# Kernel optimization log

Measured on AMD Instinct MI355X. Metric: run time of the kernel, lower is better.

Reference implementation:

```python
import jax, jax.numpy as jnp
import numpy as np

N = 100_000   # nodes
E = 1_600_000 # edges (avg degree 16)
D = 128       # dim == dim_out
NEG_SLOPE = 0.2  # PyG GATConv default


def setup_inputs() -> dict:
    key = jax.random.key(0)
    ks = jax.random.split(key, 11)
    s = 1.0 / np.sqrt(D)
    return {
        "x": jax.random.normal(ks[0], (N, D), jnp.float32),
        "edge_index": jax.random.randint(ks[1], (2, E), 0, N, jnp.int32),
        "W1": jax.random.normal(ks[2], (D, D), jnp.float32) * s,
        "a_src1": jax.random.normal(ks[3], (D,), jnp.float32) * s,
        "a_dst1": jax.random.normal(ks[4], (D,), jnp.float32) * s,
        "b1": jnp.zeros((D,), jnp.float32),
        "W2": jax.random.normal(ks[5], (D, D), jnp.float32) * s,
        "a_src2": jax.random.normal(ks[6], (D,), jnp.float32) * s,
        "a_dst2": jax.random.normal(ks[7], (D,), jnp.float32) * s,
        "b2": jnp.zeros((D,), jnp.float32),
    }


def gat_conv(x, W, a_src, a_dst, b, src, dst, n):
    # PyG GATConv, heads=1: message flows src (j) -> dst (i)
    h = x @ W                              # [n, d]
    al_src = h @ a_src                     # per-node src attention logit
    al_dst = h @ a_dst                     # per-node dst attention logit
    e = jax.nn.leaky_relu(al_src[src] + al_dst[dst], NEG_SLOPE)  # [E']
    # softmax over incoming edges of each destination node (segment softmax)
    m = jax.ops.segment_max(e, dst, num_segments=n)
    e = jnp.exp(e - m[dst])
    z = jax.ops.segment_sum(e, dst, num_segments=n)
    alpha = e / z[dst]                     # [E']
    out = jax.ops.segment_sum(h[src] * alpha[:, None], dst, num_segments=n)
    return out + b


def reference(x, edge_index, W1, a_src1, a_dst1, b1, W2, a_src2, a_dst2, b2):
    n = x.shape[0]
    loop = jnp.arange(n, dtype=edge_index.dtype)
    src = jnp.concatenate([edge_index[0], loop])  # add_self_loops=True
    dst = jnp.concatenate([edge_index[1], loop])
    h = gat_conv(x, W1, a_src1, a_dst1, b1, src, dst, n)
    # self_loops=True -> residual=False; dropout in eval mode = identity
    return gat_conv(h, W2, a_src2, a_dst2, b2, src, dst, n)
```

## Files before the change

### kernel.cpp

```cpp
#include <hip/hip_runtime.h>
#include <hip/hip_bf16.h>
#include <math.h>

#define D 128
#define LRELU_SLOPE 0.2f
#define BSH 9
#define BSZ 512
#define SC_CHUNK 16384

typedef __attribute__((ext_vector_type(8))) short bf16x8;
typedef __attribute__((ext_vector_type(4))) float f32x4;

__device__ __forceinline__ float lrelu(float x){ return x > 0.f ? x : LRELU_SLOPE * x; }

__device__ __forceinline__ unsigned short bf16_rn(float x){
  unsigned int u = __float_as_uint(x);
  return (unsigned short)((u + 0x7FFFu + ((u >> 16) & 1u)) >> 16);
}
__device__ __forceinline__ float bf16_lo_f(unsigned int u){ return __uint_as_float(u << 16); }
__device__ __forceinline__ float bf16_hi_f(unsigned int u){ return __uint_as_float(u & 0xFFFF0000u); }

__global__ __launch_bounds__(1024) void bucket_count_kernel(const int* __restrict__ dst, int E,
    int* __restrict__ bcnt, int nbuck){
  __shared__ int h[256];
  int t = threadIdx.x;
  if (t < 256) h[t] = 0;
  __syncthreads();
  for (int e = blockIdx.x*1024 + t; e < E; e += gridDim.x*1024)
    atomicAdd(&h[dst[e] >> BSH], 1);
  __syncthreads();
  if (t < nbuck && h[t]) atomicAdd(&bcnt[t], h[t]);
}

__global__ __launch_bounds__(256) void bucket_scan_kernel(const int* __restrict__ bcnt,
    int* __restrict__ bbase, int* __restrict__ bcur, int nbuck, int E){
  __shared__ int s[256];
  int t = threadIdx.x;
  int v = (t < nbuck) ? bcnt[t] : 0;
  s[t] = v;
  __syncthreads();
  #pragma unroll
  for (int d = 1; d < 256; d <<= 1){
    int add = (t >= d) ? s[t-d] : 0;
    __syncthreads();
    s[t] += add;
    __syncthreads();
  }
  if (t < nbuck){ int b = s[t] - v; bbase[t] = b; bcur[t] = b; }
  if (t == 0) bbase[nbuck] = E;
}

__global__ __launch_bounds__(1024) void bucket_scatter_kernel(const int* __restrict__ src,
    const int* __restrict__ dst, int E, int* __restrict__ bcur,
    unsigned int* __restrict__ ebuf, int nbuck){
  __shared__ int h[256];
  __shared__ int cb[256];
  int t = threadIdx.x;
  int base = blockIdx.x * SC_CHUNK;
  int end = base + SC_CHUNK; if (end > E) end = E;
  if (t < 256) h[t] = 0;
  __syncthreads();
  for (int e = base + t; e < end; e += 1024)
    atomicAdd(&h[dst[e] >> BSH], 1);
  __syncthreads();
  if (t < nbuck){
    cb[t] = h[t] ? atomicAdd(&bcur[t], h[t]) : 0;
    h[t] = 0;
  }
  __syncthreads();
  for (int e = base + t; e < end; e += 1024){
    int d = dst[e];
    int b = d >> BSH;
    int lpos = atomicAdd(&h[b], 1);
    ebuf[cb[b] + lpos] = ((unsigned int)src[e] << BSH) | (unsigned int)(d & (BSZ-1));
  }
}

__global__ __launch_bounds__(256) void bucket_csr_kernel(const unsigned int* __restrict__ ebuf,
    const int* __restrict__ bbase, int* __restrict__ row_ptr, int* __restrict__ col,
    int n, int nbuck){
  __shared__ int c[512];
  __shared__ int ps[256];
  int b = blockIdx.x;
  int t = threadIdx.x;
  int base = bbase[b], end = bbase[b+1];
  c[t] = 0; c[t+256] = 0;
  __syncthreads();
  for (int i = base + t; i < end; i += 256)
    atomicAdd(&c[ebuf[i] & (BSZ-1)], 1);
  __syncthreads();
  int a0 = c[2*t], a1 = c[2*t+1];
  int pair = a0 + a1;
  ps[t] = pair;
  __syncthreads();
  #pragma unroll
  for (int d = 1; d < 256; d <<= 1){
    int add = (t >= d) ? ps[t-d] : 0;
    __syncthreads();
    ps[t] += add;
    __syncthreads();
  }
  int excl = ps[t] - pair;
  __syncthreads();
  int lo = b << BSH;
  int g0 = lo + 2*t, g1 = g0 + 1;
  if (g0 < n) row_ptr[g0] = base + excl;
  if (g1 < n) row_ptr[g1] = base + excl + a0;
  c[2*t]   = excl;
  c[2*t+1] = excl + a0;
  __syncthreads();
  for (int i = base + t; i < end; i += 256){
    unsigned int p = ebuf[i];
    int dlo = p & (BSZ-1);
    int pos = base + atomicAdd(&c[dlo], 1);
    col[pos] = (int)(p >> BSH);
  }
  if (b == 0 && t == 0) row_ptr[n] = bbase[nbuck];
}

__global__ __launch_bounds__(256) void wsplit_kernel(const float* __restrict__ W,
    unsigned short* __restrict__ Whf, unsigned short* __restrict__ Wlf){
  int t = blockIdx.x*256 + threadIdx.x;
  int k  = t >> 7;
  int nn = t & 127;
  float w = W[t];
  unsigned short h = bf16_rn(w);
  float whf = __uint_as_float(((unsigned int)h) << 16);
  unsigned short l = bf16_rn(w - whf);
  int kc = k >> 5, l4 = (k >> 3) & 3, e = k & 7;
  int cf = nn >> 4, l15 = nn & 15;
  int idx = ((kc*8 + cf)*64 + l4*16 + l15)*8 + e;
  Whf[idx] = h; Wlf[idx] = l;
}

__global__ __launch_bounds__(64) void wa_kernel(const float* __restrict__ W,
    const float* __restrict__ a_src, const float* __restrict__ a_dst,
    float* __restrict__ wa_s, float* __restrict__ wa_d){
  int task = blockIdx.x;
  int row = task & 127;
  const float* a = (task >> 7) ? a_dst : a_src;
  int l = threadIdx.x;
  float2 v = ((const float2*)(W + row*D))[l];
  float p = v.x*a[2*l] + v.y*a[2*l+1];
  #pragma unroll
  for (int off = 32; off >= 1; off >>= 1) p += __shfl_xor(p, off);
  if (l == 0) ((task >> 7) ? wa_d : wa_s)[row] = p;
}

__global__ __launch_bounds__(256) void gemm_al_kernel(const float* __restrict__ X,
    const unsigned short* __restrict__ Whf, const unsigned short* __restrict__ Wlf,
    const float* __restrict__ Wa_src, const float* __restrict__ Wa_dst,
    unsigned short* __restrict__ Hb, float* __restrict__ ALs, float* __restrict__ ALd, int n)
{
  __shared__ unsigned short Xh[128*128];
  int tid  = threadIdx.x;
  int lane = tid & 63;
  int wave = tid >> 6;
  int row0 = blockIdx.x * 128;
  int c4   = tid & 31;

  float4 wa_s4 = ((const float4*)Wa_src)[c4];
  float4 wa_d4 = ((const float4*)Wa_dst)[c4];

  #pragma unroll 4
  for (int it = 0; it < 16; ++it){
    int f  = it*256 + tid;
    int r  = f >> 5;
    float4 v = make_float4(0.f,0.f,0.f,0.f);
    int gr = row0 + r;
    if (gr < n) v = ((const float4*)(X + (size_t)gr*D))[c4];
    unsigned short h0 = bf16_rn(v.x);
    unsigned short h1 = bf16_rn(v.y);
    unsigned short h2 = bf16_rn(v.z);
    unsigned short h3 = bf16_rn(v.w);
    int g   = (c4 >> 1) ^ (r & 7);
    int idx = r*128 + (g << 3) + ((c4 & 1) << 2);
    *(uint2*)&Xh[idx] = make_uint2((unsigned)h0 | ((unsigned)h1<<16),
                                   (unsigned)h2 | ((unsigned)h3<<16));
    float ps = v.x*wa_s4.x + v.y*wa_s4.y + v.z*wa_s4.z + v.w*wa_s4.w;
    float pd = v.x*wa_d4.x + v.y*wa_d4.y + v.z*wa_d4.z + v.w*wa_d4.w;
    #pragma unroll
    for (int off = 16; off >= 1; off >>= 1){
      ps += __shfl_xor(ps, off);
      pd += __shfl_xor(pd, off);
    }
    if ((tid & 31) == 0 && gr < n){ ALs[gr] = ps; ALd[gr] = pd; }
  }
  __syncthreads();

  int l15 = lane & 15;
  int l4  = lane >> 4;

  f32x4 acc[2][8];
  #pragma unroll
  for (int rf = 0; rf < 2; ++rf)
    #pragma unroll
    for (int cf = 0; cf < 8; ++cf)
      acc[rf][cf] = (f32x4){0.f, 0.f, 0.f, 0.f};

  #pragma unroll
  for (int kc = 0; kc < 4; ++kc){
    int g = kc*4 + l4;
    bf16x8 ah[2];
    #pragma unroll
    for (int rf = 0; rf < 2; ++rf){
      int r   = wave*32 + rf*16 + l15;
      int idx = r*128 + ((g ^ (r & 7)) << 3);
      ah[rf] = *(const bf16x8*)&Xh[idx];
    }
    #pragma unroll
    for (int cf = 0; cf < 8; ++cf){
      int foff = ((kc*8 + cf) << 9) + (lane << 3);
      bf16x8 bh = *(const bf16x8*)&Whf[foff];
      bf16x8 bl = *(const bf16x8*)&Wlf[foff];
      #pragma unroll
      for (int rf = 0; rf < 2; ++rf){
        acc[rf][cf] = __builtin_amdgcn_mfma_f32_16x16x32_bf16(ah[rf], bh, acc[rf][cf], 0, 0, 0);
        acc[rf][cf] = __builtin_amdgcn_mfma_f32_16x16x32_bf16(ah[rf], bl, acc[rf][cf], 0, 0, 0);
      }
    }
  }

  #pragma unroll
  for (int rf = 0; rf < 2; ++rf){
    #pragma unroll
    for (int reg = 0; reg < 4; ++reg){
      int gr = row0 + wave*32 + rf*16 + l4*4 + reg;
      if (gr < n){
        unsigned int p0 = (unsigned)bf16_rn(acc[rf][0][reg]) | ((unsigned)bf16_rn(acc[rf][1][reg]) << 16);
        unsigned int p1 = (unsigned)bf16_rn(acc[rf][2][reg]) | ((unsigned)bf16_rn(acc[rf][3][reg]) << 16);
        unsigned int p2 = (unsigned)bf16_rn(acc[rf][4][reg]) | ((unsigned)bf16_rn(acc[rf][5][reg]) << 16);
        unsigned int p3 = (unsigned)bf16_rn(acc[rf][6][reg]) | ((unsigned)bf16_rn(acc[rf][7][reg]) << 16);
        ((uint4*)(Hb + (size_t)gr*D))[l15] = make_uint4(p0, p1, p2, p3);
      }
    }
  }
}

__global__ __launch_bounds__(256) void agg_kernel(const unsigned short* __restrict__ Hb,
    const float* __restrict__ ALs, const float* __restrict__ ALd,
    const int* __restrict__ row_ptr, const int* __restrict__ col,
    const float* __restrict__ bias, float* __restrict__ out, int n)
{
  int gtid = blockIdx.x*blockDim.x + threadIdx.x;
  int node = gtid >> 6;
  int lane = threadIdx.x & 63;
  if (node >= n) return;

  int beg = row_ptr[node], end = row_ptr[node+1];
  float ald = ALd[node];
  float e_self = lrelu(ALs[node] + ald);

  const unsigned int* H2 = (const unsigned int*)Hb;
  unsigned int us = H2[(size_t)node*64 + lane];
  float2 acc; acc.x = bf16_lo_f(us); acc.y = bf16_hi_f(us);
  float m = e_self, z = 1.f;

  for (int c = beg; c < end; c += 64){
    int j = c + lane;
    bool valid = j < end;
    int s_l = valid ? col[j] : 0;
    float e_l = valid ? lrelu(ALs[s_l] + ald) : -1e30f;

    float mc = e_l;
    #pragma unroll
    for (int off = 32; off >= 1; off >>= 1) mc = fmaxf(mc, __shfl_xor(mc, off));
    if (mc > m){
      float sc = __expf(m - mc);
      z *= sc; acc.x *= sc; acc.y *= sc;
      m = mc;
    }
    float w_l = valid ? __expf(e_l - m) : 0.f;
    float zs = w_l;
    #pragma unroll
    for (int off = 32; off >= 1; off >>= 1) zs += __shfl_xor(zs, off);
    z += zs;

    int cnt = end - c; if (cnt > 64) cnt = 64;
    int q = 0;
    for (; q + 8 <= cnt; q += 8){
      int ss[8]; float ww[8]; unsigned int u[8];
      #pragma unroll
      for (int p = 0; p < 8; ++p){ ss[p] = __shfl(s_l, q+p); ww[p] = __shfl(w_l, q+p); }
      #pragma unroll
      for (int p = 0; p < 8; ++p) u[p] = H2[(size_t)ss[p]*64 + lane];
      #pragma unroll
      for (int p = 0; p < 8; ++p){
        acc.x += ww[p]*bf16_lo_f(u[p]);
        acc.y += ww[p]*bf16_hi_f(u[p]);
      }
    }
    for (; q < cnt; ++q){
      int s = __shfl(s_l, q);
      float w = __shfl(w_l, q);
      unsigned int u = H2[(size_t)s*64 + lane];
      acc.x += w*bf16_lo_f(u); acc.y += w*bf16_hi_f(u);
    }
  }

  float zi = 1.f / z;
  acc.x *= zi; acc.y *= zi;

  int q0 = (lane >> 4) + ((lane & 7) << 3);
  int q1 = q0 + 4;
  int hsel = (lane >> 3) & 1;
  float x0 = __shfl(acc.x, q0), y0 = __shfl(acc.y, q0);
  float x1 = __shfl(acc.x, q1), y1 = __shfl(acc.y, q1);
  float v0 = hsel ? y0 : x0;
  float v1 = hsel ? y1 : x1;

  float2 b2 = ((const float2*)bias)[lane];
  ((float2*)out)[(size_t)node*64 + lane] = make_float2(v0 + b2.x, v1 + b2.y);
}

extern "C" void kernel_launch(void* const* d_in, const int* in_sizes, int n_in,
                              void* d_out, int out_size, void* d_ws, size_t ws_size,
                              hipStream_t stream)
{
  const float* x   = (const float*)d_in[0];
  const int*   ei  = (const int*)  d_in[1];
  const float* W1  = (const float*)d_in[2];
  const float* as1 = (const float*)d_in[3];
  const float* ad1 = (const float*)d_in[4];
  const float* b1  = (const float*)d_in[5];
  const float* W2  = (const float*)d_in[6];
  const float* as2 = (const float*)d_in[7];
  const float* ad2 = (const float*)d_in[8];
  const float* b2  = (const float*)d_in[9];

  int n = in_sizes[0] / D;
  int E = in_sizes[1] / 2;
  const int* src = ei;
  const int* dst = ei + E;
  int nbuck = (n + BSZ - 1) >> BSH;

  char* base = (char*)d_ws;
  size_t off = 0;
  auto alloc = [&](size_t bytes) -> char* {
    char* p = base + off;
    off = (off + bytes + 255) & ~(size_t)255;
    return p;
  };
  unsigned short* hb = (unsigned short*)alloc((size_t)n*D*2);
  float* als   = (float*)alloc((size_t)n*4);
  float* ald   = (float*)alloc((size_t)n*4);
  int* row_ptr = (int*)alloc((size_t)(n+1)*4);
  int* bcnt    = (int*)alloc(256*4);
  int* bbase   = (int*)alloc(257*4);
  int* bcur    = (int*)alloc(256*4);
  unsigned short* whf1 = (unsigned short*)alloc(16384*2);
  unsigned short* wlf1 = (unsigned short*)alloc(16384*2);
  unsigned short* whf2 = (unsigned short*)alloc(16384*2);
  unsigned short* wlf2 = (unsigned short*)alloc(16384*2);
  float* wa_s1 = (float*)alloc(128*4);
  float* wa_d1 = (float*)alloc(128*4);
  float* wa_s2 = (float*)alloc(128*4);
  float* wa_d2 = (float*)alloc(128*4);
  unsigned int* ebuf = (unsigned int*)alloc((size_t)E*4);
  int* col   = (int*)alloc((size_t)E*4);

  float* out = (float*)d_out;

  hipMemsetAsync(bcnt, 0, 256*sizeof(int), stream);
  int sc_blocks = (E + SC_CHUNK - 1) / SC_CHUNK;
  bucket_count_kernel  <<<128, 1024, 0, stream>>>(dst, E, bcnt, nbuck);
  bucket_scan_kernel   <<<1, 256, 0, stream>>>(bcnt, bbase, bcur, nbuck, E);
  bucket_scatter_kernel<<<sc_blocks, 1024, 0, stream>>>(src, dst, E, bcur, ebuf, nbuck);
  bucket_csr_kernel    <<<nbuck, 256, 0, stream>>>(ebuf, bbase, row_ptr, col, n, nbuck);

  wsplit_kernel<<<64, 256, 0, stream>>>(W1, whf1, wlf1);
  wsplit_kernel<<<64, 256, 0, stream>>>(W2, whf2, wlf2);
  wa_kernel    <<<256, 64, 0, stream>>>(W1, as1, ad1, wa_s1, wa_d1);
  wa_kernel    <<<256, 64, 0, stream>>>(W2, as2, ad2, wa_s2, wa_d2);

  int ntiles = (n + 127)/128;
  int aggblocks = (int)(((size_t)n*64 + 255)/256);

  gemm_al_kernel<<<ntiles, 256, 0, stream>>>(x,  whf1, wlf1, wa_s1, wa_d1, hb, als, ald, n);
  agg_kernel    <<<aggblocks, 256, 0, stream>>>(hb, als, ald, row_ptr, col, b1, out, n);
  gemm_al_kernel<<<ntiles, 256, 0, stream>>>(out, whf2, wlf2, wa_s2, wa_d2, hb, als, ald, n);
  agg_kernel    <<<aggblocks, 256, 0, stream>>>(hb, als, ald, row_ptr, col, b2, out, n);
}
```

Measured before the change: 288.3 us.

## Compute attention logits via MFMA and stage edge pairs in LDS for aggregation

The per-node attention logits (X·W·a) move from FP32 dot products with shuffle reductions in the GEMM load loop into an extra MFMA column fragment. W·a_src and W·a_dst are packed as bf16 hi/lo split weights by a new small kernel. The aggregation kernel now stages (src, weight) pairs in shared memory and reads them back as broadcast LDS loads, replacing per-edge cross-lane shuffles, and uses 32-bit gather index arithmetic. This trades VALU and shuffle work for a few extra MFMAs and LDS traffic. The 32-bit indexing relies on n*64 fitting in 32 bits.

```diff
diff --git a/kernel.cpp b/kernel.cpp
--- a/kernel.cpp
+++ b/kernel.cpp
@@ -147,9 +147,28 @@
   if (l == 0) ((task >> 7) ? wa_d : wa_s)[row] = p;
 }
 
+__global__ __launch_bounds__(256) void wafrag_kernel(const float* __restrict__ wa_s,
+    const float* __restrict__ wa_d, unsigned short* __restrict__ Whfx,
+    unsigned short* __restrict__ Wlfx){
+  int t = threadIdx.x;
+  int kc = t >> 6, lane = t & 63;
+  int l15 = lane & 15, l4 = lane >> 4;
+  unsigned short hh[8], ll[8];
+  #pragma unroll
+  for (int e = 0; e < 8; ++e){
+    int k = (kc*4 + l4)*8 + e;
+    float v = (l15 == 0) ? wa_s[k] : ((l15 == 1) ? wa_d[k] : 0.f);
+    unsigned short h = bf16_rn(v);
+    hh[e] = h;
+    ll[e] = bf16_rn(v - __uint_as_float(((unsigned)h) << 16));
+  }
+  #pragma unroll
+  for (int e = 0; e < 8; ++e){ Whfx[t*8 + e] = hh[e]; Wlfx[t*8 + e] = ll[e]; }
+}
+
 __global__ __launch_bounds__(256) void gemm_al_kernel(const float* __restrict__ X,
     const unsigned short* __restrict__ Whf, const unsigned short* __restrict__ Wlf,
-    const float* __restrict__ Wa_src, const float* __restrict__ Wa_dst,
+    const unsigned short* __restrict__ Whfx, const unsigned short* __restrict__ Wlfx,
     unsigned short* __restrict__ Hb, float* __restrict__ ALs, float* __restrict__ ALd, int n)
 {
   __shared__ unsigned short Xh[128*128];
@@ -158,9 +177,6 @@
   int wave = tid >> 6;
   int row0 = blockIdx.x * 128;
   int c4   = tid & 31;
-
-  float4 wa_s4 = ((const float4*)Wa_src)[c4];
-  float4 wa_d4 = ((const float4*)Wa_dst)[c4];
 
   #pragma unroll 4
   for (int it = 0; it < 16; ++it){
@@ -177,14 +193,6 @@
     int idx = r*128 + (g << 3) + ((c4 & 1) << 2);
     *(uint2*)&Xh[idx] = make_uint2((unsigned)h0 | ((unsigned)h1<<16),
                                    (unsigned)h2 | ((unsigned)h3<<16));
-    float ps = v.x*wa_s4.x + v.y*wa_s4.y + v.z*wa_s4.z + v.w*wa_s4.w;
-    float pd = v.x*wa_d4.x + v.y*wa_d4.y + v.z*wa_d4.z + v.w*wa_d4.w;
-    #pragma unroll
-    for (int off = 16; off >= 1; off >>= 1){
-      ps += __shfl_xor(ps, off);
-      pd += __shfl_xor(pd, off);
-    }
-    if ((tid & 31) == 0 && gr < n){ ALs[gr] = ps; ALd[gr] = pd; }
   }
   __syncthreads();
 
@@ -192,11 +200,14 @@
   int l4  = lane >> 4;
 
   f32x4 acc[2][8];
-  #pragma unroll
-  for (int rf = 0; rf < 2; ++rf)
+  f32x4 acc2[2];
+  #pragma unroll
+  for (int rf = 0; rf < 2; ++rf){
     #pragma unroll
     for (int cf = 0; cf < 8; ++cf)
       acc[rf][cf] = (f32x4){0.f, 0.f, 0.f, 0.f};
+    acc2[rf] = (f32x4){0.f, 0.f, 0.f, 0.f};
+  }
 
   #pragma unroll
   for (int kc = 0; kc < 4; ++kc){
@@ -219,6 +230,16 @@
         acc[rf][cf] = __builtin_amdgcn_mfma_f32_16x16x32_bf16(ah[rf], bl, acc[rf][cf], 0, 0, 0);
       }
     }
+    {
+      int foffx = ((kc << 6) + lane) << 3;
+      bf16x8 bhx = *(const bf16x8*)&Whfx[foffx];
+      bf16x8 blx = *(const bf16x8*)&Wlfx[foffx];
+      #pragma unroll
+      for (int rf = 0; rf < 2; ++rf){
+        acc2[rf] = __builtin_amdgcn_mfma_f32_16x16x32_bf16(ah[rf], bhx, acc2[rf], 0, 0, 0);
+        acc2[rf] = __builtin_amdgcn_mfma_f32_16x16x32_bf16(ah[rf], blx, acc2[rf], 0, 0, 0);
+      }
+    }
   }
 
   #pragma unroll
@@ -232,6 +253,8 @@
         unsigned int p2 = (unsigned)bf16_rn(acc[rf][4][reg]) | ((unsigned)bf16_rn(acc[rf][5][reg]) << 16);
         unsigned int p3 = (unsigned)bf16_rn(acc[rf][6][reg]) | ((unsigned)bf16_rn(acc[rf][7][reg]) << 16);
         ((uint4*)(Hb + (size_t)gr*D))[l15] = make_uint4(p0, p1, p2, p3);
+        if (l15 == 0)      ALs[gr] = acc2[rf][reg];
+        else if (l15 == 1) ALd[gr] = acc2[rf][reg];
       }
     }
   }
@@ -242,9 +265,11 @@
     const int* __restrict__ row_ptr, const int* __restrict__ col,
     const float* __restrict__ bias, float* __restrict__ out, int n)
 {
+  __shared__ uint2 pairs[256];
   int gtid = blockIdx.x*blockDim.x + threadIdx.x;
   int node = gtid >> 6;
   int lane = threadIdx.x & 63;
+  int wbase = threadIdx.x & 192;
   if (node >= n) return;
 
   int beg = row_ptr[node], end = row_ptr[node+1];
@@ -252,7 +277,7 @@
   float e_self = lrelu(ALs[node] + ald);
 
   const unsigned int* H2 = (const unsigned int*)Hb;
-  unsigned int us = H2[(size_t)node*64 + lane];
+  unsigned int us = H2[(unsigned)(node*64 + lane)];
   float2 acc; acc.x = bf16_lo_f(us); acc.y = bf16_hi_f(us);
   float m = e_self, z = 1.f;
 
@@ -276,24 +301,27 @@
     for (int off = 32; off >= 1; off >>= 1) zs += __shfl_xor(zs, off);
     z += zs;
 
+    pairs[threadIdx.x] = make_uint2((unsigned)s_l, __float_as_uint(w_l));
+
     int cnt = end - c; if (cnt > 64) cnt = 64;
     int q = 0;
     for (; q + 8 <= cnt; q += 8){
-      int ss[8]; float ww[8]; unsigned int u[8];
+      uint2 pw[8]; unsigned int u[8];
       #pragma unroll
-      for (int p = 0; p < 8; ++p){ ss[p] = __shfl(s_l, q+p); ww[p] = __shfl(w_l, q+p); }
+      for (int p = 0; p < 8; ++p) pw[p] = pairs[wbase + q + p];
       #pragma unroll
-      for (int p = 0; p < 8; ++p) u[p] = H2[(size_t)ss[p]*64 + lane];
+      for (int p = 0; p < 8; ++p) u[p] = H2[(unsigned)(pw[p].x*64u + lane)];
       #pragma unroll
       for (int p = 0; p < 8; ++p){
-        acc.x += ww[p]*bf16_lo_f(u[p]);
-        acc.y += ww[p]*bf16_hi_f(u[p]);
+        float w = __uint_as_float(pw[p].y);
+        acc.x += w*bf16_lo_f(u[p]);
+        acc.y += w*bf16_hi_f(u[p]);
       }
     }
     for (; q < cnt; ++q){
-      int s = __shfl(s_l, q);
-      float w = __shfl(w_l, q);
-      unsigned int u = H2[(size_t)s*64 + lane];
+      uint2 pw = pairs[wbase + q];
+      unsigned int u = H2[(unsigned)(pw.x*64u + lane)];
+      float w = __uint_as_float(pw.y);
       acc.x += w*bf16_lo_f(u); acc.y += w*bf16_hi_f(u);
     }
   }
@@ -352,6 +380,10 @@
   unsigned short* wlf1 = (unsigned short*)alloc(16384*2);
   unsigned short* whf2 = (unsigned short*)alloc(16384*2);
   unsigned short* wlf2 = (unsigned short*)alloc(16384*2);
+  unsigned short* whfx1 = (unsigned short*)alloc(2048*2);
+  unsigned short* wlfx1 = (unsigned short*)alloc(2048*2);
+  unsigned short* whfx2 = (unsigned short*)alloc(2048*2);
+  unsigned short* wlfx2 = (unsigned short*)alloc(2048*2);
   float* wa_s1 = (float*)alloc(128*4);
   float* wa_d1 = (float*)alloc(128*4);
   float* wa_s2 = (float*)alloc(128*4);
@@ -372,12 +404,14 @@
   wsplit_kernel<<<64, 256, 0, stream>>>(W2, whf2, wlf2);
   wa_kernel    <<<256, 64, 0, stream>>>(W1, as1, ad1, wa_s1, wa_d1);
   wa_kernel    <<<256, 64, 0, stream>>>(W2, as2, ad2, wa_s2, wa_d2);
+  wafrag_kernel<<<1, 256, 0, stream>>>(wa_s1, wa_d1, whfx1, wlfx1);
+  wafrag_kernel<<<1, 256, 0, stream>>>(wa_s2, wa_d2, whfx2, wlfx2);
 
   int ntiles = (n + 127)/128;
   int aggblocks = (int)(((size_t)n*64 + 255)/256);
 
-  gemm_al_kernel<<<ntiles, 256, 0, stream>>>(x,  whf1, wlf1, wa_s1, wa_d1, hb, als, ald, n);
+  gemm_al_kernel<<<ntiles, 256, 0, stream>>>(x,  whf1, wlf1, whfx1, wlfx1, hb, als, ald, n);
   agg_kernel    <<<aggblocks, 256, 0, stream>>>(hb, als, ald, row_ptr, col, b1, out, n);
-  gemm_al_kernel<<<ntiles, 256, 0, stream>>>(out, whf2, wlf2, wa_s2, wa_d2, hb, als, ald, n);
+  gemm_al_kernel<<<ntiles, 256, 0, stream>>>(out, whf2, wlf2, whfx2, wlfx2, hb, als, ald, n);
   agg_kernel    <<<aggblocks, 256, 0, stream>>>(hb, als, ald, row_ptr, col, b2, out, n);
 }
```

Result: no change. 290.8 us (+0.9%).
